# Kernel tuning notes

Measured on AMD Instinct MI355X. Metric: run time of the kernel, lower is better.

Reference implementation:

```python
import jax, jax.numpy as jnp
import numpy as np

EPS = 1e-6
STRIDE = 2  # kv_pool_stride
NUM_HEADS = 8

def _layernorm(x, w, b):
    mu = jnp.mean(x, axis=-1, keepdims=True)
    var = jnp.mean(jnp.square(x - mu), axis=-1, keepdims=True)
    return (x - mu) * jax.lax.rsqrt(var + EPS) * w + b

def setup_inputs() -> dict:
    key = jax.random.key(0)
    B, H, W, C = 8, 56, 56, 384
    hidden = int(C * 2.0)
    ks = jax.random.split(key, 12)
    s = 0.02
    return {
        "x": jax.random.normal(ks[0], (B, H * W, C), jnp.float32),
        "ln1_w": jnp.ones((C,), jnp.float32),
        "ln1_b": jnp.zeros((C,), jnp.float32),
        "qw": jax.random.normal(ks[1], (C, C), jnp.float32) * s,
        "qb": jnp.zeros((C,), jnp.float32),
        "kw": jax.random.normal(ks[2], (C, C), jnp.float32) * s,
        "kb": jnp.zeros((C,), jnp.float32),
        "vw": jax.random.normal(ks[3], (C, C), jnp.float32) * s,
        "vb": jnp.zeros((C,), jnp.float32),
        "pw": jax.random.normal(ks[4], (C, C), jnp.float32) * s,
        "pb": jnp.zeros((C,), jnp.float32),
        "ln2_w": jnp.ones((C,), jnp.float32),
        "ln2_b": jnp.zeros((C,), jnp.float32),
        "fc1_w": jax.random.normal(ks[5], (C, hidden), jnp.float32) * s,
        "fc1_b": jnp.zeros((hidden,), jnp.float32),
        "fc2_w": jax.random.normal(ks[6], (hidden, C), jnp.float32) * s,
        "fc2_b": jnp.zeros((C,), jnp.float32),
        "H": 56,
        "W": 56,
    }

def reference(x, ln1_w, ln1_b, qw, qb, kw, kb, vw, vb, pw, pb,
              ln2_w, ln2_b, fc1_w, fc1_b, fc2_w, fc2_b, H, W):
    B, N, C = x.shape
    h = NUM_HEADS
    d = C // h
    scale = d ** -0.5

    # Attention branch: Q from norm1(x); K,V from RAW x (as in source), KV avg-pooled 2x2
    q_tok = _layernorm(x, ln1_w, ln1_b)
    s = STRIDE
    Hk, Wk = H // s, W // s
    kv = x.reshape(B, Hk, s, Wk, s, C).mean(axis=(2, 4)).reshape(B, Hk * Wk, C)

    q = (q_tok @ qw + qb).reshape(B, N, h, d)
    k = (kv @ kw + kb).reshape(B, Hk * Wk, h, d)
    v = (kv @ vw + vb).reshape(B, Hk * Wk, h, d)

    attn = jnp.einsum('bqhd,bkhd->bhqk', q, k) * scale
    attn = jax.nn.softmax(attn, axis=-1)
    out = jnp.einsum('bhqk,bkhd->bqhd', attn, v).reshape(B, N, C)
    x = x + (out @ pw + pb)

    # MLP branch (GELU exact, matching torch nn.GELU default)
    y = _layernorm(x, ln2_w, ln2_b)
    y = jax.nn.gelu(y @ fc1_w + fc1_b, approximate=False)
    x = x + (y @ fc2_w + fc2_b)
    return x
```

## Files before the change

### kernel.cpp

```cpp
#include <hip/hip_runtime.h>
#include <math.h>

#define B_    8
#define N_TOK 3136
#define C_    384
#define DH    48
#define NK    784
#define HID   768
#define M1    25088
#define M2    6272
#define M1Q   6272

typedef unsigned short u16;
typedef __attribute__((ext_vector_type(8))) short bf16x8;
typedef __attribute__((ext_vector_type(4))) float f32x4;

__device__ __forceinline__ float b2f(u16 u) {
  return __uint_as_float(((unsigned)u) << 16);
}
__device__ __forceinline__ u16 f2b(float f) {
  unsigned u = __float_as_uint(f);
  return (u16)((u + 0x7fffu + ((u >> 16) & 1u)) >> 16);
}
__device__ __forceinline__ u16 f2b_trunc(float f) {
  return (u16)(__float_as_uint(f) >> 16);
}
__device__ __forceinline__ void gload_lds16(const u16* g, u16* l) {
  __builtin_amdgcn_global_load_lds(
      (const __attribute__((address_space(1))) void*)g,
      (__attribute__((address_space(3))) void*)l, 16, 0, 0);
}

__global__ __launch_bounds__(256) void ln1_pool(
    const float* __restrict__ X, const float* __restrict__ w,
    const float* __restrict__ b, u16* __restrict__ Y, u16* __restrict__ KV) {
  if (blockIdx.x < M1 / 4) {
    const int row = blockIdx.x * 4 + (threadIdx.x >> 6);
    const int lane = threadIdx.x & 63;
    const size_t base = (size_t)row * C_;
    float v[6];
#pragma unroll
    for (int i = 0; i < 6; ++i) v[i] = X[base + lane + 64 * i];
    float s = 0.f;
#pragma unroll
    for (int i = 0; i < 6; ++i) s += v[i];
#pragma unroll
    for (int off = 32; off > 0; off >>= 1) s += __shfl_xor(s, off);
    const float mu = s * (1.0f / C_);
    float q = 0.f;
#pragma unroll
    for (int i = 0; i < 6; ++i) { float d = v[i] - mu; q += d * d; }
#pragma unroll
    for (int off = 32; off > 0; off >>= 1) q += __shfl_xor(q, off);
    const float r = rsqrtf(q * (1.0f / C_) + 1e-6f);
#pragma unroll
    for (int i = 0; i < 6; ++i) {
      int c = lane + 64 * i;
      Y[base + c] = f2b((v[i] - mu) * r * w[c] + b[c]);
    }
  } else {
    int t = (blockIdx.x - M1 / 4) * 256 + threadIdx.x;
    if (t >= M2 * C_) return;
    int c = t % C_;
    int row = t / C_;
    int bb = row / NK;
    int rr = row - bb * NK;
    int hk = rr / 28;
    int wk = rr - hk * 28;
    const float* p = X + ((size_t)(bb * N_TOK + hk * 112 + wk * 2)) * C_ + c;
    KV[t] = f2b(0.25f * (p[0] + p[C_] + p[56 * C_] + p[57 * C_]));
  }
}

__global__ __launch_bounds__(256) void ln2_rows(const u16* __restrict__ X,
    const float* __restrict__ w, const float* __restrict__ b, u16* __restrict__ Y) {
  const int row = blockIdx.x * 4 + (threadIdx.x >> 6);
  const int lane = threadIdx.x & 63;
  const size_t base = (size_t)row * C_;
  float v[6];
#pragma unroll
  for (int i = 0; i < 6; ++i) v[i] = b2f(X[base + lane + 64 * i]);
  float s = 0.f;
#pragma unroll
  for (int i = 0; i < 6; ++i) s += v[i];
#pragma unroll
  for (int off = 32; off > 0; off >>= 1) s += __shfl_xor(s, off);
  const float mu = s * (1.0f / C_);
  float q = 0.f;
#pragma unroll
  for (int i = 0; i < 6; ++i) { float d = v[i] - mu; q += d * d; }
#pragma unroll
  for (int off = 32; off > 0; off >>= 1) q += __shfl_xor(q, off);
  const float r = rsqrtf(q * (1.0f / C_) + 1e-6f);
#pragma unroll
  for (int i = 0; i < 6; ++i) {
    int c = lane + 64 * i;
    Y[base + c] = f2b((v[i] - mu) * r * w[c] + b[c]);
  }
}

struct TransArgs {
  const float* src[6];
  u16* dst[6];
  int K[6], N[6], tx[6], ty[6];
};
__global__ __launch_bounds__(256) void transpose_all(TransArgs a) {
  const int id = blockIdx.z;
  if ((int)blockIdx.x >= a.tx[id] || (int)blockIdx.y >= a.ty[id]) return;
  const float* W = a.src[id];
  u16* WT = a.dst[id];
  const int K = a.K[id], N = a.N[id];
  __shared__ u16 tile[64][73];
  const int k0 = blockIdx.y * 64, n0 = blockIdx.x * 64;
  for (int i = threadIdx.x; i < 64 * 64; i += 256) {
    int kk = i >> 6, nn = i & 63;
    tile[kk][nn] = f2b(W[(size_t)(k0 + kk) * N + n0 + nn]);
  }
  __syncthreads();
  for (int i = threadIdx.x; i < 64 * 64; i += 256) {
    int nn = i >> 6, kk = i & 63;
    WT[(size_t)(n0 + nn) * K + k0 + kk] = tile[kk][nn];
  }
}

template<int EPI, bool RES32, bool OUT32>
__device__ __forceinline__ void gemm_core(
    const u16* __restrict__ A, const u16* __restrict__ BT,
    const float* __restrict__ bias, const void* __restrict__ resv,
    void* __restrict__ Cv, int N, int K, int m0, int n0) {
  __shared__ u16 As[128 * 64];
  __shared__ u16 Bs[128 * 64];
  const int tid  = threadIdx.x;
  const int wave = tid >> 6;
  const int lane = tid & 63;
  const int quad = lane >> 4;
  const int ll   = lane & 15;
  const int wm   = wave >> 1, wn = wave & 1;

  const int srow = wave * 32 + (lane >> 3);
  const int sgs  = lane & 7;

  f32x4 acc[4][4];
#pragma unroll
  for (int i = 0; i < 4; ++i)
#pragma unroll
    for (int j = 0; j < 4; ++j) acc[i][j] = (f32x4){0.f, 0.f, 0.f, 0.f};

  for (int kk0 = 0; kk0 < K; kk0 += 64) {
    __syncthreads();
#pragma unroll
    for (int c = 0; c < 4; ++c) {
      const int r = srow + c * 8;
      const int g = sgs ^ (r & 7);
      gload_lds16(A  + (size_t)(m0 + r) * K + kk0 + g * 8,
                  As + (size_t)(wave * 32 + c * 8) * 64);
      gload_lds16(BT + (size_t)(n0 + r) * K + kk0 + g * 8,
                  Bs + (size_t)(wave * 32 + c * 8) * 64);
    }
    __syncthreads();
#pragma unroll
    for (int ks = 0; ks < 2; ++ks) {
      const int gsw = (quad + 4 * ks) ^ (ll & 7);
      bf16x8 af[4], bfr[4];
#pragma unroll
      for (int im = 0; im < 4; ++im)
        af[im] = *(const bf16x8*)&As[(size_t)(wm * 64 + im * 16 + ll) * 64 + gsw * 8];
#pragma unroll
      for (int jn = 0; jn < 4; ++jn)
        bfr[jn] = *(const bf16x8*)&Bs[(size_t)(wn * 64 + jn * 16 + ll) * 64 + gsw * 8];
#pragma unroll
      for (int im = 0; im < 4; ++im)
#pragma unroll
        for (int jn = 0; jn < 4; ++jn)
          acc[im][jn] = __builtin_amdgcn_mfma_f32_16x16x32_bf16(
              af[im], bfr[jn], acc[im][jn], 0, 0, 0);
    }
  }

  float bb[4];
#pragma unroll
  for (int jn = 0; jn < 4; ++jn) bb[jn] = bias[n0 + wn * 64 + jn * 16 + ll];
#pragma unroll
  for (int im = 0; im < 4; ++im) {
    const int row = m0 + wm * 64 + im * 16 + quad * 4;
#pragma unroll
    for (int jn = 0; jn < 4; ++jn) {
      const int col = n0 + wn * 64 + jn * 16 + ll;
#pragma unroll
      for (int r = 0; r < 4; ++r) {
        float o = acc[im][jn][r] + bb[jn];
        if (EPI == 1) {
          o = 0.5f * o * (1.0f + erff(o * 0.70710678118654752f));
        } else if (EPI == 2) {
          size_t ri = (size_t)(row + r) * N + col;
          o += RES32 ? ((const float*)resv)[ri] : b2f(((const u16*)resv)[ri]);
        }
        if (OUT32) ((float*)Cv)[(size_t)(row + r) * N + col] = o;
        else       ((u16*)Cv)[(size_t)(row + r) * N + col] = f2b(o);
      }
    }
  }
}

template<int EPI, bool RES32, bool OUT32>
__global__ __launch_bounds__(256) void gemm_bt(
    const u16* __restrict__ A, const u16* __restrict__ BT,
    const float* __restrict__ bias, const void* __restrict__ resv,
    void* __restrict__ Cv, int N, int K) {
  gemm_core<EPI, RES32, OUT32>(A, BT, bias, resv, Cv, N, K,
                               blockIdx.y << 7, blockIdx.x << 7);
}

struct QKVArgs {
  const u16* A[3];
  const u16* BT[3];
  const float* bias[3];
  u16* C[3];
  int M[3];
};
__global__ __launch_bounds__(256) void gemm_qkv(QKVArgs a) {
  const int z = blockIdx.z;
  const int m0 = blockIdx.y << 7;
  if (m0 >= a.M[z]) return;
  gemm_core<0, false, false>(a.A[z], a.BT[z], a.bias[z], nullptr, a.C[z],
                             C_, C_, m0, blockIdx.x << 7);
}

#define QS_STR 72
__global__ __launch_bounds__(512) void attn_mfma(
    const u16* __restrict__ Q, const u16* __restrict__ Kb,
    const u16* __restrict__ Vb, u16* __restrict__ O) {
  __shared__ u16 Qs[128 * QS_STR];
  __shared__ u16 Ks[64 * QS_STR];
  __shared__ u16 Vt[48 * QS_STR];
  __shared__ u16 Ps[128 * QS_STR];
  const int tid  = threadIdx.x;
  const int wave = tid >> 6;
  const int lane = tid & 63;
  const int quad = lane >> 4;
  const int ll   = lane & 15;
  const int qt   = blockIdx.x;
  const int bh   = blockIdx.y;
  const int b    = bh >> 3, h = bh & 7;
  const int q0   = qt * 128;
  const float scale = 0.14433756729740643f;

  for (int i = tid; i < 128 * 16; i += 512) {
    int r = i >> 4, c = i & 15;
    Qs[r * QS_STR + 48 + c] = 0;
    if (r < 64) Ks[r * QS_STR + 48 + c] = 0;
  }
  {
    const int part = tid & 7;
#pragma unroll
    for (int it = 0; it < 2; ++it) {
      const int row = it * 64 + (tid >> 3);
      if (part < 6) {
        const int qrow = q0 + row;
        if (qrow < N_TOK) {
          uint4 v = *(const uint4*)(Q + ((size_t)(b * N_TOK) + qrow) * C_ + h * DH + part * 8);
          const u16* vp = (const u16*)&v;
          u16 ov[8];
#pragma unroll
          for (int j = 0; j < 8; ++j) ov[j] = f2b(b2f(vp[j]) * scale);
          *(uint4*)&Qs[row * QS_STR + part * 8] = *(const uint4*)ov;
        } else {
          uint4 z = {0, 0, 0, 0};
          *(uint4*)&Qs[row * QS_STR + part * 8] = z;
        }
      }
    }
  }

  f32x4 Ofr[3] = {{0.f,0.f,0.f,0.f},{0.f,0.f,0.f,0.f},{0.f,0.f,0.f,0.f}};
  float lrow[4] = {0.f, 0.f, 0.f, 0.f};

  for (int t = 0; t < 13; ++t) {
    const int kbase = t * 64;
    __syncthreads();
    {
      const int key = tid >> 3, part = tid & 7;
      if (part < 6 && kbase + key < NK) {
        uint4 v = *(const uint4*)(Kb + ((size_t)(b * NK) + kbase + key) * C_ + h * DH + part * 8);
        *(uint4*)&Ks[key * QS_STR + part * 8] = v;
      }
    }
    {
      const int part = tid >> 6, key = tid & 63;
      if (part < 6 && kbase + key < NK) {
        uint4 v = *(const uint4*)(Vb + ((size_t)(b * NK) + kbase + key) * C_ + h * DH + part * 8);
        const u16* vp = (const u16*)&v;
#pragma unroll
        for (int j = 0; j < 8; ++j)
          Vt[(part * 8 + j) * QS_STR + key] = vp[j];
      }
    }
    __syncthreads();

    f32x4 S[4];
#pragma unroll
    for (int nt = 0; nt < 4; ++nt) {
      f32x4 acc = {0.f, 0.f, 0.f, 0.f};
#pragma unroll
      for (int k0 = 0; k0 < 64; k0 += 32) {
        bf16x8 a = *(const bf16x8*)&Qs[(wave * 16 + ll) * QS_STR + k0 + quad * 8];
        bf16x8 bb = *(const bf16x8*)&Ks[(nt * 16 + ll) * QS_STR + k0 + quad * 8];
        acc = __builtin_amdgcn_mfma_f32_16x16x32_bf16(a, bb, acc, 0, 0, 0);
      }
      if (kbase + nt * 16 + ll >= NK)
        acc = (f32x4){-1e30f, -1e30f, -1e30f, -1e30f};
      S[nt] = acc;
    }
#pragma unroll
    for (int nt = 0; nt < 4; ++nt) {
      const int g = nt * 2 + (ll >> 3);
      const int gp = g ^ quad;
#pragma unroll
      for (int r = 0; r < 4; ++r) {
        float p = __expf(S[nt][r]);
        lrow[r] += p;
        Ps[(wave * 16 + quad * 4 + r) * QS_STR + (gp << 3) + (ll & 7)] = f2b_trunc(p);
      }
    }
#pragma unroll
    for (int dt = 0; dt < 3; ++dt)
#pragma unroll
      for (int ks = 0; ks < 2; ++ks) {
        const int gp = ((ks << 2) + quad) ^ ((ll >> 2) & 3);
        bf16x8 a = *(const bf16x8*)&Ps[(wave * 16 + ll) * QS_STR + (gp << 3)];
        bf16x8 bb = *(const bf16x8*)&Vt[(dt * 16 + ll) * QS_STR + ks * 32 + quad * 8];
        Ofr[dt] = __builtin_amdgcn_mfma_f32_16x16x32_bf16(a, bb, Ofr[dt], 0, 0, 0);
      }
  }
#pragma unroll
  for (int msk = 1; msk < 16; msk <<= 1)
#pragma unroll
    for (int r = 0; r < 4; ++r)
      lrow[r] += __shfl_xor(lrow[r], msk);
  float inv[4];
#pragma unroll
  for (int r = 0; r < 4; ++r) inv[r] = 1.0f / lrow[r];
#pragma unroll
  for (int dt = 0; dt < 3; ++dt)
#pragma unroll
    for (int r = 0; r < 4; ++r) {
      int qrow = q0 + wave * 16 + quad * 4 + r;
      if (qrow < N_TOK)
        O[((size_t)b * N_TOK + qrow) * C_ + h * DH + dt * 16 + ll] =
            f2b(Ofr[dt][r] * inv[r]);
    }
}

__global__ __launch_bounds__(256) void marker_fill(
    float* __restrict__ out, size_t n, float val) {
  size_t i = (size_t)blockIdx.x * 256 + threadIdx.x;
  const size_t stride = (size_t)gridDim.x * 256;
  for (; i < n; i += stride) out[i] = 0.f;
  if (blockIdx.x == 0 && threadIdx.x == 0) out[0] = val;
}

extern "C" void kernel_launch(void* const* d_in, const int* in_sizes, int n_in,
                              void* d_out, int out_size, void* d_ws, size_t ws_size,
                              hipStream_t stream) {
  const float* x    = (const float*)d_in[0];
  const float* ln1w = (const float*)d_in[1];
  const float* ln1b = (const float*)d_in[2];
  const float* qw   = (const float*)d_in[3];
  const float* qb   = (const float*)d_in[4];
  const float* kw   = (const float*)d_in[5];
  const float* kb   = (const float*)d_in[6];
  const float* vw   = (const float*)d_in[7];
  const float* vb   = (const float*)d_in[8];
  const float* pw   = (const float*)d_in[9];
  const float* pb   = (const float*)d_in[10];
  const float* ln2w = (const float*)d_in[11];
  const float* ln2b = (const float*)d_in[12];
  const float* fc1w = (const float*)d_in[13];
  const float* fc1b = (const float*)d_in[14];
  const float* fc2w = (const float*)d_in[15];
  const float* fc2b = (const float*)d_in[16];

  const size_t BUF = (size_t)M1 * C_;
  float* outf = (float*)d_out;

  {
    static const int exp_sizes[19] = {
      M1 * C_, C_, C_, C_ * C_, C_, C_ * C_, C_, C_ * C_, C_, C_ * C_, C_,
      C_, C_, C_ * HID, HID, HID * C_, C_, 1, 1};
    int bad = -1;
    if (n_in != 19) bad = 99;
    else {
      for (int i = 0; i < 19; ++i)
        if (in_sizes[i] != exp_sizes[i]) { bad = i; break; }
    }
    if (bad >= 0) {
      marker_fill<<<1024, 256, 0, stream>>>(outf, BUF, 10000.0f + (float)bad);
      return;
    }
  }
  const size_t need_min  = 4096 + 3 * BUF * sizeof(u16);
  const size_t need_full = 4096 + (3 * BUF + (size_t)M1 * HID) * sizeof(u16);
  if (ws_size < need_min) {
    marker_fill<<<1024, 256, 0, stream>>>(outf, BUF, 30000.0f + (float)(ws_size >> 20));
    return;
  }
  const bool full_mlp = (ws_size >= need_full);

  u16* T0 = (u16*)((char*)d_ws + 4096);
  u16* T1 = T0 + BUF;
  u16* U  = T1 + BUF;
  u16* P  = U;
  u16* KB = U + (size_t)M2 * C_;
  u16* VB = U + (size_t)2 * M2 * C_;
  u16* HBq = U;
  u16* HBfull = U + BUF;
  u16* WTb = U + BUF - (size_t)(4 * C_ * C_ + 2 * C_ * HID);
  u16* wtq = WTb;
  u16* wtk = wtq + C_ * C_;
  u16* wtv = wtk + C_ * C_;
  u16* wtp = wtv + C_ * C_;
  u16* wtf1 = wtp + C_ * C_;
  u16* wtf2 = wtf1 + (size_t)C_ * HID;

  {
    TransArgs ta;
    ta.src[0] = qw;   ta.dst[0] = wtq;  ta.K[0] = C_;  ta.N[0] = C_;  ta.tx[0] = 6;  ta.ty[0] = 6;
    ta.src[1] = kw;   ta.dst[1] = wtk;  ta.K[1] = C_;  ta.N[1] = C_;  ta.tx[1] = 6;  ta.ty[1] = 6;
    ta.src[2] = vw;   ta.dst[2] = wtv;  ta.K[2] = C_;  ta.N[2] = C_;  ta.tx[2] = 6;  ta.ty[2] = 6;
    ta.src[3] = pw;   ta.dst[3] = wtp;  ta.K[3] = C_;  ta.N[3] = C_;  ta.tx[3] = 6;  ta.ty[3] = 6;
    ta.src[4] = fc1w; ta.dst[4] = wtf1; ta.K[4] = C_;  ta.N[4] = HID; ta.tx[4] = 12; ta.ty[4] = 6;
    ta.src[5] = fc2w; ta.dst[5] = wtf2; ta.K[5] = HID; ta.N[5] = C_;  ta.tx[5] = 6;  ta.ty[5] = 12;
    transpose_all<<<dim3(12, 12, 6), 256, 0, stream>>>(ta);
  }

  ln1_pool<<<M1 / 4 + (M2 * C_) / 256, 256, 0, stream>>>(x, ln1w, ln1b, T0, P);

  {
    QKVArgs qa;
    qa.A[0] = T0; qa.BT[0] = wtq; qa.bias[0] = qb; qa.C[0] = T1; qa.M[0] = M1;
    qa.A[1] = P;  qa.BT[1] = wtk; qa.bias[1] = kb; qa.C[1] = KB; qa.M[1] = M2;
    qa.A[2] = P;  qa.BT[2] = wtv; qa.bias[2] = vb; qa.C[2] = VB; qa.M[2] = M2;
    gemm_qkv<<<dim3(3, 196, 3), 256, 0, stream>>>(qa);
  }

  attn_mfma<<<dim3(25, 64), 512, 0, stream>>>(T1, KB, VB, T0);

  gemm_bt<2, true, false><<<dim3(3, 196), 256, 0, stream>>>(
      T0, wtp, pb, x, T1, C_, C_);

  ln2_rows<<<M1 / 4, 256, 0, stream>>>(T1, ln2w, ln2b, T0);

  if (full_mlp) {
    gemm_bt<1, false, false><<<dim3(6, 196), 256, 0, stream>>>(
        T0, wtf1, fc1b, nullptr, HBfull, HID, C_);
    gemm_bt<2, false, true><<<dim3(3, 196), 256, 0, stream>>>(
        HBfull, wtf2, fc2b, T1, outf, C_, HID);
  } else {
    for (int qtr = 0; qtr < 4; ++qtr) {
      const size_t ro = (size_t)qtr * M1Q;
      gemm_bt<1, false, false><<<dim3(6, 49), 256, 0, stream>>>(
          T0 + ro * C_, wtf1, fc1b, nullptr, HBq, HID, C_);
      gemm_bt<2, false, true><<<dim3(3, 49), 256, 0, stream>>>(
          HBq, wtf2, fc2b, T1 + ro * C_, outf + ro * C_, C_, HID);
    }
  }
}
```

Baseline: 349.1 us.

## Double-buffer K/V tiles in attention and keep Q fragments in registers

Restructures the attention kernel to double-buffer the K and V shared-memory tiles. The next tile's K is loaded directly to LDS and its V is held in registers while MFMAs run on the current tile, which removes one barrier per iteration. Q is loaded straight into register fragments instead of being staged through shared memory. The softmax scale moves from a per-element pre-scale of Q into the exponent, and K uses an XOR-swizzled layout without padding. In exchange it uses more LDS for the double buffers and holds extra registers for the prefetched V.

```diff
diff --git a/kernel.cpp b/kernel.cpp
--- a/kernel.cpp
+++ b/kernel.cpp
@@ -230,9 +230,8 @@
 __global__ __launch_bounds__(512) void attn_mfma(
     const u16* __restrict__ Q, const u16* __restrict__ Kb,
     const u16* __restrict__ Vb, u16* __restrict__ O) {
-  __shared__ u16 Qs[128 * QS_STR];
-  __shared__ u16 Ks[64 * QS_STR];
-  __shared__ u16 Vt[48 * QS_STR];
+  __shared__ u16 Ks[2][64 * 64];
+  __shared__ u16 Vt[2][48 * QS_STR];
   __shared__ u16 Ps[128 * QS_STR];
   const int tid  = threadIdx.x;
   const int wave = tid >> 6;
@@ -245,93 +244,98 @@
   const int q0   = qt * 128;
   const float scale = 0.14433756729740643f;
 
-  for (int i = tid; i < 128 * 16; i += 512) {
-    int r = i >> 4, c = i & 15;
-    Qs[r * QS_STR + 48 + c] = 0;
-    if (r < 64) Ks[r * QS_STR + 48 + c] = 0;
-  }
+  bf16x8 af0, af1;
   {
-    const int part = tid & 7;
-#pragma unroll
-    for (int it = 0; it < 2; ++it) {
-      const int row = it * 64 + (tid >> 3);
-      if (part < 6) {
-        const int qrow = q0 + row;
-        if (qrow < N_TOK) {
-          uint4 v = *(const uint4*)(Q + ((size_t)(b * N_TOK) + qrow) * C_ + h * DH + part * 8);
-          const u16* vp = (const u16*)&v;
-          u16 ov[8];
-#pragma unroll
-          for (int j = 0; j < 8; ++j) ov[j] = f2b(b2f(vp[j]) * scale);
-          *(uint4*)&Qs[row * QS_STR + part * 8] = *(const uint4*)ov;
-        } else {
-          uint4 z = {0, 0, 0, 0};
-          *(uint4*)&Qs[row * QS_STR + part * 8] = z;
-        }
-      }
-    }
-  }
+    int qrow = q0 + wave * 16 + ll;
+    if (qrow >= N_TOK) qrow = N_TOK - 1;
+    const u16* qp = Q + ((size_t)(b * N_TOK) + qrow) * C_ + h * DH;
+    af0 = *(const bf16x8*)(qp + quad * 8);
+    if (quad < 2) af1 = *(const bf16x8*)(qp + 32 + quad * 8);
+    else          af1 = (bf16x8){0, 0, 0, 0, 0, 0, 0, 0};
+  }
+
+  const int krow = (wave << 3) + (lane >> 3);
+  const int kgrp = (lane & 7) ^ (lane >> 3);
+  const size_t kbase_g = (size_t)(b * NK) * C_ + h * DH + kgrp * 8;
+
+  uint4 vreg;
+
+  {
+    int kk = krow; if (kk >= NK) kk = NK - 1;
+    gload_lds16(Kb + kbase_g + (size_t)kk * C_, &Ks[0][wave << 9]);
+    if (wave < 6) {
+      int vk = lane; if (vk >= NK) vk = NK - 1;
+      vreg = *(const uint4*)(Vb + ((size_t)(b * NK) + vk) * C_ + h * DH + wave * 8);
+      const u16* vp = (const u16*)&vreg;
+#pragma unroll
+      for (int j = 0; j < 8; ++j)
+        Vt[0][(wave * 8 + j) * QS_STR + lane] = vp[j];
+    }
+  }
+  __syncthreads();
 
   f32x4 Ofr[3] = {{0.f,0.f,0.f,0.f},{0.f,0.f,0.f,0.f},{0.f,0.f,0.f,0.f}};
   float lrow[4] = {0.f, 0.f, 0.f, 0.f};
 
   for (int t = 0; t < 13; ++t) {
+    const int cur = t & 1, nxt = cur ^ 1;
     const int kbase = t * 64;
-    __syncthreads();
-    {
-      const int key = tid >> 3, part = tid & 7;
-      if (part < 6 && kbase + key < NK) {
-        uint4 v = *(const uint4*)(Kb + ((size_t)(b * NK) + kbase + key) * C_ + h * DH + part * 8);
-        *(uint4*)&Ks[key * QS_STR + part * 8] = v;
+
+    if (t < 12) {
+      const int knext = kbase + 64;
+      int kk = knext + krow; if (kk >= NK) kk = NK - 1;
+      gload_lds16(Kb + kbase_g + (size_t)kk * C_, &Ks[nxt][wave << 9]);
+      if (wave < 6) {
+        int vk = knext + lane; if (vk >= NK) vk = NK - 1;
+        vreg = *(const uint4*)(Vb + ((size_t)(b * NK) + vk) * C_ + h * DH + wave * 8);
       }
     }
-    {
-      const int part = tid >> 6, key = tid & 63;
-      if (part < 6 && kbase + key < NK) {
-        uint4 v = *(const uint4*)(Vb + ((size_t)(b * NK) + kbase + key) * C_ + h * DH + part * 8);
-        const u16* vp = (const u16*)&v;
-#pragma unroll
-        for (int j = 0; j < 8; ++j)
-          Vt[(part * 8 + j) * QS_STR + key] = vp[j];
-      }
-    }
-    __syncthreads();
 
     f32x4 S[4];
 #pragma unroll
     for (int nt = 0; nt < 4; ++nt) {
+      const int rb = (nt * 16 + ll) * 64;
+      bf16x8 b0 = *(const bf16x8*)&Ks[cur][rb + ((quad    ) ^ (ll & 7)) * 8];
+      bf16x8 b1 = *(const bf16x8*)&Ks[cur][rb + ((quad + 4) ^ (ll & 7)) * 8];
       f32x4 acc = {0.f, 0.f, 0.f, 0.f};
-#pragma unroll
-      for (int k0 = 0; k0 < 64; k0 += 32) {
-        bf16x8 a = *(const bf16x8*)&Qs[(wave * 16 + ll) * QS_STR + k0 + quad * 8];
-        bf16x8 bb = *(const bf16x8*)&Ks[(nt * 16 + ll) * QS_STR + k0 + quad * 8];
-        acc = __builtin_amdgcn_mfma_f32_16x16x32_bf16(a, bb, acc, 0, 0, 0);
-      }
+      acc = __builtin_amdgcn_mfma_f32_16x16x32_bf16(af0, b0, acc, 0, 0, 0);
+      acc = __builtin_amdgcn_mfma_f32_16x16x32_bf16(af1, b1, acc, 0, 0, 0);
       if (kbase + nt * 16 + ll >= NK)
         acc = (f32x4){-1e30f, -1e30f, -1e30f, -1e30f};
       S[nt] = acc;
     }
+
 #pragma unroll
     for (int nt = 0; nt < 4; ++nt) {
       const int g = nt * 2 + (ll >> 3);
       const int gp = g ^ quad;
 #pragma unroll
       for (int r = 0; r < 4; ++r) {
-        float p = __expf(S[nt][r]);
+        float p = __expf(S[nt][r] * scale);
         lrow[r] += p;
         Ps[(wave * 16 + quad * 4 + r) * QS_STR + (gp << 3) + (ll & 7)] = f2b_trunc(p);
       }
     }
+
 #pragma unroll
     for (int dt = 0; dt < 3; ++dt)
 #pragma unroll
       for (int ks = 0; ks < 2; ++ks) {
         const int gp = ((ks << 2) + quad) ^ ((ll >> 2) & 3);
         bf16x8 a = *(const bf16x8*)&Ps[(wave * 16 + ll) * QS_STR + (gp << 3)];
-        bf16x8 bb = *(const bf16x8*)&Vt[(dt * 16 + ll) * QS_STR + ks * 32 + quad * 8];
+        bf16x8 bb = *(const bf16x8*)&Vt[cur][(dt * 16 + ll) * QS_STR + ks * 32 + quad * 8];
         Ofr[dt] = __builtin_amdgcn_mfma_f32_16x16x32_bf16(a, bb, Ofr[dt], 0, 0, 0);
       }
-  }
+
+    if (t < 12 && wave < 6) {
+      const u16* vp = (const u16*)&vreg;
+#pragma unroll
+      for (int j = 0; j < 8; ++j)
+        Vt[nxt][(wave * 8 + j) * QS_STR + lane] = vp[j];
+    }
+    __syncthreads();
+  }
+
 #pragma unroll
   for (int msk = 1; msk < 16; msk <<= 1)
 #pragma unroll
```

New measurement: 343.4 us. About the same (-1.6%).
